# Optimization experiments

Hardware: AMD Instinct MI355X
Metric: run time of the kernel (lower is better)

Reference implementation:

```python
import jax, jax.numpy as jnp
import numpy as np

N_NODES = 100000
N_EDGES = 1600000
IN_DIM, HIDDEN_DIM, OUT_DIM = 64, 128, 40


def setup_inputs() -> dict:
    key = jax.random.key(0)
    k1, k2, k3, k4 = jax.random.split(key, 4)
    x = jax.random.normal(k1, (N_NODES, IN_DIM), dtype=jnp.float32)
    edge_index = jax.random.randint(k2, (2, N_EDGES), 0, N_NODES, dtype=jnp.int64)
    W1 = jax.random.normal(k3, (IN_DIM, HIDDEN_DIM), dtype=jnp.float32) * 0.05
    b1 = jnp.zeros((HIDDEN_DIM,), dtype=jnp.float32)
    W2 = jax.random.normal(k4, (HIDDEN_DIM, OUT_DIM), dtype=jnp.float32) * 0.05
    b2 = jnp.zeros((OUT_DIM,), dtype=jnp.float32)
    return {"x": x, "edge_index": edge_index, "W1": W1, "b1": b1, "W2": W2, "b2": b2}


def reference(x, edge_index, W1, b1, W2, b2):
    # PyG GINConv with default eps=0: out = nn(x_i + sum_{j in N(i)} x_j)
    src = edge_index[0]
    dst = edge_index[1]
    n = x.shape[0]

    def gin_layer(h, W, b):
        aggr = jax.ops.segment_sum(h[src], dst, num_segments=n)  # scatter-add of neighbor feats
        return (h + aggr) @ W + b

    h = jax.nn.relu(gin_layer(x, W1, b1))
    # dropout is identity in eval mode (training=False)
    h = gin_layer(h, W2, b2)
    return jax.nn.log_softmax(h, axis=1)
```

## Files before the change

### kernel.cpp

```cpp
#include <hip/hip_runtime.h>
#include <math.h>


#define IN_DIM 64
#define HID_DIM 128
#define OUT_DIM 40

#define BSH 8
#define MAXNB 512
#define EPB 4096
#define CAP 5120
#define H1S 136
#define EPT 16
#define CPT 20

typedef unsigned short ushort;
typedef unsigned char uchar;
typedef unsigned int uint;
typedef float floatx2 __attribute__((ext_vector_type(2)));
typedef short short8_t __attribute__((ext_vector_type(8)));
typedef float float4_t __attribute__((ext_vector_type(4)));

__device__ __forceinline__ ushort f2bf(float f) {
  unsigned u = __float_as_uint(f);
  u += 0x7fffu + ((u >> 16) & 1u);
  return (ushort)(u >> 16);
}


__global__ __launch_bounds__(256) void prep(
    const float4* __restrict__ x4, uint2* __restrict__ x8, int n8,
    const float* __restrict__ W1, const float* __restrict__ W2,
    ushort* __restrict__ W1T, ushort* __restrict__ W2T, int* __restrict__ gcur) {
  int id = blockIdx.x * 256 + threadIdx.x;
  if (id < n8) {
    float4 a = x4[2 * id], b = x4[2 * id + 1];
    int p0 = __builtin_amdgcn_cvt_pk_fp8_f32(a.x, a.y, 0, false);
    p0 = __builtin_amdgcn_cvt_pk_fp8_f32(a.z, a.w, p0, true);
    int p1 = __builtin_amdgcn_cvt_pk_fp8_f32(b.x, b.y, 0, false);
    p1 = __builtin_amdgcn_cvt_pk_fp8_f32(b.z, b.w, p1, true);
    x8[id] = (uint2){(uint)p0, (uint)p1};
  }
  if (id < HID_DIM * IN_DIM) {
    int c = id / IN_DIM, k = id - c * IN_DIM;
    W1T[id] = f2bf(W1[k * HID_DIM + c]);
  }
  if (id < 48 * HID_DIM) {
    int c = id / HID_DIM, k = id - c * HID_DIM;
    W2T[id] = (c < OUT_DIM) ? f2bf(W2[k * OUT_DIM + c]) : 0;
  }
  if (id < MAXNB) gcur[id] = 0;
}


__global__ __launch_bounds__(256) void bucket_scatter(
    const int* __restrict__ src, const int* __restrict__ dst,
    int* __restrict__ gcur, int* __restrict__ epk_s, int n_edges, int nb) {
  __shared__ int hist[MAXNB];
  __shared__ int lexcl[MAXNB];
  __shared__ int lofs[MAXNB];
  __shared__ int gbase[MAXNB];
  __shared__ int spk[EPB];
  __shared__ ushort sbid[EPB];
  int tid = threadIdx.x;
  for (int i = tid; i < nb; i += 256) { hist[i] = 0; lofs[i] = 0; }
  __syncthreads();
  int e0 = blockIdx.x * EPB;
  int cnt = min(EPB, n_edges - e0);
  int dr[EPT], sr[EPT];
#pragma unroll
  for (int r = 0; r < EPT; ++r) {
    int i = r * 256 + tid;
    if (i < cnt) {
      dr[r] = dst[e0 + i];
      sr[r] = src[e0 + i];
      atomicAdd(&hist[dr[r] >> BSH], 1);
    } else { dr[r] = -1; sr[r] = 0; }
  }
  __syncthreads();
  if (tid < 64) {
    int carry = 0;
    for (int c = 0; c < nb; c += 64) {
      int v = (c + tid < nb) ? hist[c + tid] : 0;
      int incl = v;
#pragma unroll
      for (int d = 1; d < 64; d <<= 1) {
        int t = __shfl_up(incl, d, 64);
        if (tid >= d) incl += t;
      }
      if (c + tid < nb) lexcl[c + tid] = carry + incl - v;
      carry += __shfl(incl, 63, 64);
    }
  }
  __syncthreads();
  for (int i = tid; i < nb; i += 256)
    if (hist[i]) gbase[i] = atomicAdd(&gcur[i], hist[i]);
  __syncthreads();
#pragma unroll
  for (int r = 0; r < EPT; ++r) {
    if (dr[r] >= 0) {
      int b = dr[r] >> BSH;
      int p = lexcl[b] + atomicAdd(&lofs[b], 1);
      spk[p] = ((dr[r] & 255) << 17) | sr[r];
      sbid[p] = (ushort)b;
    }
  }
  __syncthreads();
  for (int i = tid; i < cnt; i += 256) {
    int b = sbid[i];
    epk_s[b * CAP + gbase[b] + (i - lexcl[b])] = spk[i];
  }
}


__global__ __launch_bounds__(256) void bucket_csr(
    const int* __restrict__ epk_s, const int* __restrict__ gcnt,
    int2* __restrict__ off2, int* __restrict__ esrc_s, int n_nodes) {
  __shared__ int hist[256];
  __shared__ int cur[256];
  int b = blockIdx.x;
  int base = b * CAP;
  int cnt = gcnt[b];
  int nb0 = b << BSH;
  int nn = min(256, n_nodes - nb0);
  int tid = threadIdx.x;
  hist[tid] = 0;
  __syncthreads();
  int pv[CPT];
#pragma unroll
  for (int r = 0; r < CPT; ++r) {
    int i = r * 256 + tid;
    if (i < cnt) {
      pv[r] = epk_s[base + i];
      atomicAdd(&hist[pv[r] >> 17], 1);
    } else pv[r] = -1;
  }
  __syncthreads();
  if (tid < 64) {
    int carry = 0;
#pragma unroll
    for (int c = 0; c < 256; c += 64) {
      int v = hist[c + tid];
      int incl = v;
#pragma unroll
      for (int d = 1; d < 64; d <<= 1) {
        int t = __shfl_up(incl, d, 64);
        if (tid >= d) incl += t;
      }
      cur[c + tid] = carry + incl - v;
      carry += __shfl(incl, 63, 64);
    }
  }
  __syncthreads();
  if (tid < nn) {
    int st = cur[tid];
    off2[nb0 + tid] = make_int2(base + st, base + st + hist[tid]);
  }
  __syncthreads();
#pragma unroll
  for (int r = 0; r < CPT; ++r) {
    if (pv[r] >= 0) {
      int pos = atomicAdd(&cur[pv[r] >> 17], 1);
      esrc_s[base + pos] = pv[r] & 0x1FFFF;
    }
  }
}


__global__ __launch_bounds__(256) void agg1(
    const float4* __restrict__ x4, const uint2* __restrict__ x8,
    const int2* __restrict__ off2, const int* __restrict__ esrc,
    ushort* __restrict__ aggrh, int n_nodes) {
  int tid = threadIdx.x;
  int lane = tid & 63;
  int nsel = (lane >> 5) & 1, es = (lane >> 3) & 3, q = lane & 7;
  int node = blockIdx.x * 8 + (tid >> 6) * 2 + nsel;
  bool nok = node < n_nodes;
  int2 oe = nok ? off2[node] : make_int2(0, 0);
  floatx2 A0 = {0.f, 0.f}, A1 = {0.f, 0.f}, A2 = {0.f, 0.f}, A3 = {0.f, 0.f};
  floatx2 C0 = {0.f, 0.f}, C1 = {0.f, 0.f}, C2 = {0.f, 0.f}, C3 = {0.f, 0.f};
  int e = oe.x, end = oe.y;
  for (; e + 8 <= end; e += 8) {
    uint2 u0 = x8[(uint)(esrc[e + es] * 8 + q)];
    uint2 u1 = x8[(uint)(esrc[e + 4 + es] * 8 + q)];
    A0 += __builtin_amdgcn_cvt_pk_f32_fp8((int)u0.x, false);
    A1 += __builtin_amdgcn_cvt_pk_f32_fp8((int)u0.x, true);
    A2 += __builtin_amdgcn_cvt_pk_f32_fp8((int)u0.y, false);
    A3 += __builtin_amdgcn_cvt_pk_f32_fp8((int)u0.y, true);
    C0 += __builtin_amdgcn_cvt_pk_f32_fp8((int)u1.x, false);
    C1 += __builtin_amdgcn_cvt_pk_f32_fp8((int)u1.x, true);
    C2 += __builtin_amdgcn_cvt_pk_f32_fp8((int)u1.y, false);
    C3 += __builtin_amdgcn_cvt_pk_f32_fp8((int)u1.y, true);
  }
  for (; e < end; e += 4) {
    int idx = e + es;
    if (idx < end) {
      uint2 u = x8[(uint)(esrc[idx] * 8 + q)];
      A0 += __builtin_amdgcn_cvt_pk_f32_fp8((int)u.x, false);
      A1 += __builtin_amdgcn_cvt_pk_f32_fp8((int)u.x, true);
      A2 += __builtin_amdgcn_cvt_pk_f32_fp8((int)u.y, false);
      A3 += __builtin_amdgcn_cvt_pk_f32_fp8((int)u.y, true);
    }
  }
  A0 += C0; A1 += C1; A2 += C2; A3 += C3;
#pragma unroll
  for (int d = 8; d <= 16; d <<= 1) {
    floatx2 t0, t1, t2, t3;
    t0[0] = __shfl_xor(A0[0], d, 64); t0[1] = __shfl_xor(A0[1], d, 64);
    t1[0] = __shfl_xor(A1[0], d, 64); t1[1] = __shfl_xor(A1[1], d, 64);
    t2[0] = __shfl_xor(A2[0], d, 64); t2[1] = __shfl_xor(A2[1], d, 64);
    t3[0] = __shfl_xor(A3[0], d, 64); t3[1] = __shfl_xor(A3[1], d, 64);
    A0 += t0; A1 += t1; A2 += t2; A3 += t3;
  }
  if (nok) {
    float4 xa = x4[(uint)(node * 16 + q * 2)];
    float4 xb = x4[(uint)(node * 16 + q * 2 + 1)];
    A0 += (floatx2){xa.x, xa.y};
    A1 += (floatx2){xa.z, xa.w};
    A2 += (floatx2){xb.x, xb.y};
    A3 += (floatx2){xb.z, xb.w};
  }
  if (nok && es == 0) {
    uint4 o;
    o.x = (uint)f2bf(A0[0]) | ((uint)f2bf(A0[1]) << 16);
    o.y = (uint)f2bf(A1[0]) | ((uint)f2bf(A1[1]) << 16);
    o.z = (uint)f2bf(A2[0]) | ((uint)f2bf(A2[1]) << 16);
    o.w = (uint)f2bf(A3[0]) | ((uint)f2bf(A3[1]) << 16);
    ((uint4*)aggrh)[(uint)(node * 8 + q)] = o;
  }
}


__global__ __launch_bounds__(256) void gemm12_mfma(
    const ushort* __restrict__ aggrh, const ushort* __restrict__ W1T,
    const float* __restrict__ b1, const ushort* __restrict__ W2T,
    uchar* __restrict__ th8, int n_nodes) {
  __shared__ ushort h1s[64 * H1S];
  int w = threadIdx.x >> 6, lane = threadIdx.x & 63;
  int n0 = blockIdx.x * 64 + w * 16;
  int row = lane & 15, kg = lane >> 4;
  int n = n0 + row;
  {
    short8_t a0 = {}, a1 = {};
    if (n < n_nodes) {
      a0 = *(const short8_t*)&aggrh[(size_t)n * IN_DIM + kg * 8];
      a1 = *(const short8_t*)&aggrh[(size_t)n * IN_DIM + 32 + kg * 8];
    }
    float4_t acc[8];
#pragma unroll
    for (int ct = 0; ct < 8; ++ct) acc[ct] = (float4_t){0.f, 0.f, 0.f, 0.f};
#pragma unroll
    for (int ct = 0; ct < 8; ++ct) {
      int c = ct * 16 + row;
      short8_t b0 = *(const short8_t*)&W1T[(size_t)c * IN_DIM + kg * 8];
      short8_t b1f = *(const short8_t*)&W1T[(size_t)c * IN_DIM + 32 + kg * 8];
      acc[ct] = __builtin_amdgcn_mfma_f32_16x16x32_bf16(a0, b0, acc[ct], 0, 0, 0);
      acc[ct] = __builtin_amdgcn_mfma_f32_16x16x32_bf16(a1, b1f, acc[ct], 0, 0, 0);
    }
#pragma unroll
    for (int ct = 0; ct < 8; ++ct) {
      int j = ct * 16 + row;
      float bias = b1[j];
#pragma unroll
      for (int i = 0; i < 4; ++i) {
        int nl = w * 16 + kg * 4 + i;
        h1s[nl * H1S + j] = f2bf(fmaxf(acc[ct][i] + bias, 0.f));
      }
    }
  }
  __syncthreads();
  {
    short8_t a[4];
#pragma unroll
    for (int ks = 0; ks < 4; ++ks)
      a[ks] = *(const short8_t*)&h1s[(w * 16 + row) * H1S + ks * 32 + kg * 8];
    float4_t acc[3];
#pragma unroll
    for (int ct = 0; ct < 3; ++ct) acc[ct] = (float4_t){0.f, 0.f, 0.f, 0.f};
#pragma unroll
    for (int ct = 0; ct < 3; ++ct) {
      int c = ct * 16 + row;
#pragma unroll
      for (int ks = 0; ks < 4; ++ks) {
        short8_t b = *(const short8_t*)&W2T[(size_t)c * HID_DIM + ks * 32 + kg * 8];
        acc[ct] = __builtin_amdgcn_mfma_f32_16x16x32_bf16(a[ks], b, acc[ct], 0, 0, 0);
      }
    }
#pragma unroll
    for (int ct = 0; ct < 3; ++ct) {
      int j = ct * 16 + row;
      if (j < OUT_DIM) {
#pragma unroll
        for (int i = 0; i < 4; ++i) {
          int nn = n0 + kg * 4 + i;
          if (nn < n_nodes) {
            int pk = __builtin_amdgcn_cvt_pk_fp8_f32(acc[ct][i], acc[ct][i], 0, false);
            th8[(size_t)nn * 40 + j] = (uchar)(pk & 0xff);
          }
        }
      }
    }
  }
}


__global__ __launch_bounds__(256) void final_fused(
    const uchar* __restrict__ th8, const int2* __restrict__ off2,
    const int* __restrict__ esrc, const float* __restrict__ b2,
    float* __restrict__ out, int n_nodes) {
  int tid = threadIdx.x;
  int lane = tid & 63;
  int nsel = (lane >> 5) & 1, es = (lane >> 4) & 1, q = lane & 15;
  int node = blockIdx.x * 8 + (tid >> 6) * 2 + nsel;
  bool nok = node < n_nodes;
  bool valid = nok && (q < 10);
  const uint* tr = (const uint*)th8;
  int2 oe = nok ? off2[node] : make_int2(0, 0);
  uint uown = 0;
  float4 bb = {0.f, 0.f, 0.f, 0.f};
  if (valid) {
    uown = tr[(uint)(node * 10 + q)];
    bb = ((const float4*)b2)[q];
  }
  floatx2 A01 = {0.f, 0.f}, A23 = {0.f, 0.f};
  floatx2 C01 = {0.f, 0.f}, C23 = {0.f, 0.f};
  int e = oe.x, end = oe.y;
  for (; e + 8 <= end; e += 8) {
    uint u0 = 0, u1 = 0, u2 = 0, u3 = 0;
    if (valid) {
      u0 = tr[(uint)(esrc[e + es] * 10 + q)];
      u1 = tr[(uint)(esrc[e + es + 2] * 10 + q)];
      u2 = tr[(uint)(esrc[e + es + 4] * 10 + q)];
      u3 = tr[(uint)(esrc[e + es + 6] * 10 + q)];
    }
    A01 += __builtin_amdgcn_cvt_pk_f32_fp8((int)u0, false);
    A23 += __builtin_amdgcn_cvt_pk_f32_fp8((int)u0, true);
    C01 += __builtin_amdgcn_cvt_pk_f32_fp8((int)u1, false);
    C23 += __builtin_amdgcn_cvt_pk_f32_fp8((int)u1, true);
    A01 += __builtin_amdgcn_cvt_pk_f32_fp8((int)u2, false);
    A23 += __builtin_amdgcn_cvt_pk_f32_fp8((int)u2, true);
    C01 += __builtin_amdgcn_cvt_pk_f32_fp8((int)u3, false);
    C23 += __builtin_amdgcn_cvt_pk_f32_fp8((int)u3, true);
  }
  for (; e < end; e += 2) {
    int idx = e + es;
    if (idx < end && valid) {
      uint u = tr[(uint)(esrc[idx] * 10 + q)];
      A01 += __builtin_amdgcn_cvt_pk_f32_fp8((int)u, false);
      A23 += __builtin_amdgcn_cvt_pk_f32_fp8((int)u, true);
    }
  }
  A01 += C01; A23 += C23;
  {
    floatx2 t0, t1;
    t0[0] = __shfl_xor(A01[0], 16, 64); t0[1] = __shfl_xor(A01[1], 16, 64);
    t1[0] = __shfl_xor(A23[0], 16, 64); t1[1] = __shfl_xor(A23[1], 16, 64);
    A01 += t0; A23 += t1;
  }
  A01 += __builtin_amdgcn_cvt_pk_f32_fp8((int)uown, false);
  A23 += __builtin_amdgcn_cvt_pk_f32_fp8((int)uown, true);
  A01 += (floatx2){bb.x, bb.y};
  A23 += (floatx2){bb.z, bb.w};
  float m = valid ? fmaxf(fmaxf(A01[0], A01[1]), fmaxf(A23[0], A23[1])) : -INFINITY;
#pragma unroll
  for (int d = 1; d <= 8; d <<= 1) m = fmaxf(m, __shfl_xor(m, d, 64));
  float ssum = 0.f;
  if (valid)
    ssum = (__expf(A01[0] - m) + __expf(A01[1] - m)) +
           (__expf(A23[0] - m) + __expf(A23[1] - m));
#pragma unroll
  for (int d = 1; d <= 8; d <<= 1) ssum += __shfl_xor(ssum, d, 64);
  if (valid && es == 0) {
    float ls = m + __logf(ssum);
    float4 o = {A01[0] - ls, A01[1] - ls, A23[0] - ls, A23[1] - ls};
    ((float4*)out)[(uint)(node * 10 + q)] = o;
  }
}


static inline char* align256(char* p) {
  return (char*)(((uintptr_t)p + 255) & ~(uintptr_t)255);
}

extern "C" void kernel_launch(void* const* d_in, const int* in_sizes, int n_in,
                              void* d_out, int out_size, void* d_ws, size_t ws_size,
                              hipStream_t stream) {
  const float* x  = (const float*)d_in[0];
  const int*   ei = (const int*)d_in[1];
  const float* W1 = (const float*)d_in[2];
  const float* b1 = (const float*)d_in[3];
  const float* W2 = (const float*)d_in[4];
  const float* b2 = (const float*)d_in[5];
  float* out = (float*)d_out;

  int n_nodes = in_sizes[0] / IN_DIM;
  int n_edges = in_sizes[1] / 2;
  const int* src = ei;
  const int* dst = ei + n_edges;
  int nb = (n_nodes + 255) >> BSH;

  char* p = (char*)d_ws;
  int* gcur   = (int*)p;            p += MAXNB * 4;
  int2* off2  = (int2*)p;           p += (size_t)n_nodes * 8;
  p = align256(p);
  int* epk_s  = (int*)p;            p += (size_t)nb * CAP * 4;
  int* esrc_s = (int*)p;            p += (size_t)nb * CAP * 4;
  p = align256(p);
  uchar* x8    = (uchar*)p;         p += (size_t)n_nodes * IN_DIM;
  p = align256(p);
  ushort* aggrh = (ushort*)p;       p += (size_t)n_nodes * IN_DIM * 2;
  p = align256(p);
  uchar* th8    = (uchar*)p;        p += (size_t)n_nodes * 40 + 256;
  p = align256(p);
  ushort* W1T   = (ushort*)p;       p += HID_DIM * IN_DIM * 2;
  ushort* W2T   = (ushort*)p;       p += 48 * HID_DIM * 2;

  int n8 = n_nodes * IN_DIM / 8;
  prep<<<(n8 + 255) / 256, 256, 0, stream>>>(
      (const float4*)x, (uint2*)x8, n8, W1, W2, W1T, W2T, gcur);

  int egrid = (n_edges + EPB - 1) / EPB;
  bucket_scatter<<<egrid, 256, 0, stream>>>(src, dst, gcur, epk_s, n_edges, nb);
  bucket_csr<<<nb, 256, 0, stream>>>(epk_s, gcur, off2, esrc_s, n_nodes);

  agg1<<<(n_nodes + 7) / 8, 256, 0, stream>>>(
      (const float4*)x, (const uint2*)x8, off2, esrc_s, aggrh, n_nodes);
  int ggrid = (n_nodes + 63) / 64;
  gemm12_mfma<<<ggrid, 256, 0, stream>>>(aggrh, W1T, b1, W2T, th8, n_nodes);
  final_fused<<<(n_nodes + 7) / 8, 256, 0, stream>>>(th8, off2, esrc_s, b2, out, n_nodes);
}
```

Before: 138.1 us.

## Scatter bucketed edges directly to global and widen fp8 gathers in final layer

The bucket scatter kernel no longer stages edges in shared memory with a local prefix scan. It writes each packed edge straight to its global bucket slot using a per-block global base plus a shared atomic offset, which removes a scan, two barriers and the LDS staging at the cost of less coalesced global writes. The final aggregation kernel now has each lane load 8 fp8 bytes (uint2) instead of 4 and processes 4 edges in parallel per node instead of 2, so fewer lanes sit idle (5 of 8 valid instead of 10 of 16). This adds an extra shuffle reduction stage.

Measured after the change: 139.1 us. No clear change (+0.7%).

```diff
diff --git a/kernel.cpp b/kernel.cpp
--- a/kernel.cpp
+++ b/kernel.cpp
@@ -57,11 +57,8 @@
     const int* __restrict__ src, const int* __restrict__ dst,
     int* __restrict__ gcur, int* __restrict__ epk_s, int n_edges, int nb) {
   __shared__ int hist[MAXNB];
-  __shared__ int lexcl[MAXNB];
   __shared__ int lofs[MAXNB];
   __shared__ int gbase[MAXNB];
-  __shared__ int spk[EPB];
-  __shared__ ushort sbid[EPB];
   int tid = threadIdx.x;
   for (int i = tid; i < nb; i += 256) { hist[i] = 0; lofs[i] = 0; }
   __syncthreads();
@@ -78,21 +75,6 @@
     } else { dr[r] = -1; sr[r] = 0; }
   }
   __syncthreads();
-  if (tid < 64) {
-    int carry = 0;
-    for (int c = 0; c < nb; c += 64) {
-      int v = (c + tid < nb) ? hist[c + tid] : 0;
-      int incl = v;
-#pragma unroll
-      for (int d = 1; d < 64; d <<= 1) {
-        int t = __shfl_up(incl, d, 64);
-        if (tid >= d) incl += t;
-      }
-      if (c + tid < nb) lexcl[c + tid] = carry + incl - v;
-      carry += __shfl(incl, 63, 64);
-    }
-  }
-  __syncthreads();
   for (int i = tid; i < nb; i += 256)
     if (hist[i]) gbase[i] = atomicAdd(&gcur[i], hist[i]);
   __syncthreads();
@@ -100,15 +82,9 @@
   for (int r = 0; r < EPT; ++r) {
     if (dr[r] >= 0) {
       int b = dr[r] >> BSH;
-      int p = lexcl[b] + atomicAdd(&lofs[b], 1);
-      spk[p] = ((dr[r] & 255) << 17) | sr[r];
-      sbid[p] = (ushort)b;
-    }
-  }
-  __syncthreads();
-  for (int i = tid; i < cnt; i += 256) {
-    int b = sbid[i];
-    epk_s[b * CAP + gbase[b] + (i - lexcl[b])] = spk[i];
+      int p = gbase[b] + atomicAdd(&lofs[b], 1);
+      epk_s[b * CAP + p] = ((dr[r] & 255) << 17) | sr[r];
+    }
   }
 }
 
@@ -310,70 +286,84 @@
     float* __restrict__ out, int n_nodes) {
   int tid = threadIdx.x;
   int lane = tid & 63;
-  int nsel = (lane >> 5) & 1, es = (lane >> 4) & 1, q = lane & 15;
+  int nsel = (lane >> 5) & 1, es = (lane >> 3) & 3, q = lane & 7;
   int node = blockIdx.x * 8 + (tid >> 6) * 2 + nsel;
   bool nok = node < n_nodes;
-  bool valid = nok && (q < 10);
-  const uint* tr = (const uint*)th8;
+  bool valid = nok && (q < 5);
+  const uint2* tr2 = (const uint2*)th8;
   int2 oe = nok ? off2[node] : make_int2(0, 0);
-  uint uown = 0;
-  float4 bb = {0.f, 0.f, 0.f, 0.f};
+  uint2 uown = {0, 0};
+  float4 bb0 = {0.f, 0.f, 0.f, 0.f}, bb1 = {0.f, 0.f, 0.f, 0.f};
   if (valid) {
-    uown = tr[(uint)(node * 10 + q)];
-    bb = ((const float4*)b2)[q];
-  }
-  floatx2 A01 = {0.f, 0.f}, A23 = {0.f, 0.f};
-  floatx2 C01 = {0.f, 0.f}, C23 = {0.f, 0.f};
+    uown = tr2[(uint)(node * 5 + q)];
+    bb0 = ((const float4*)b2)[2 * q];
+    bb1 = ((const float4*)b2)[2 * q + 1];
+  }
+  floatx2 A0 = {0.f, 0.f}, A1 = {0.f, 0.f}, A2 = {0.f, 0.f}, A3 = {0.f, 0.f};
+  floatx2 C0 = {0.f, 0.f}, C1 = {0.f, 0.f}, C2 = {0.f, 0.f}, C3 = {0.f, 0.f};
   int e = oe.x, end = oe.y;
   for (; e + 8 <= end; e += 8) {
-    uint u0 = 0, u1 = 0, u2 = 0, u3 = 0;
+    uint2 u0 = {0, 0}, u1 = {0, 0};
     if (valid) {
-      u0 = tr[(uint)(esrc[e + es] * 10 + q)];
-      u1 = tr[(uint)(esrc[e + es + 2] * 10 + q)];
-      u2 = tr[(uint)(esrc[e + es + 4] * 10 + q)];
-      u3 = tr[(uint)(esrc[e + es + 6] * 10 + q)];
-    }
-    A01 += __builtin_amdgcn_cvt_pk_f32_fp8((int)u0, false);
-    A23 += __builtin_amdgcn_cvt_pk_f32_fp8((int)u0, true);
-    C01 += __builtin_amdgcn_cvt_pk_f32_fp8((int)u1, false);
-    C23 += __builtin_amdgcn_cvt_pk_f32_fp8((int)u1, true);
-    A01 += __builtin_amdgcn_cvt_pk_f32_fp8((int)u2, false);
-    A23 += __builtin_amdgcn_cvt_pk_f32_fp8((int)u2, true);
-    C01 += __builtin_amdgcn_cvt_pk_f32_fp8((int)u3, false);
-    C23 += __builtin_amdgcn_cvt_pk_f32_fp8((int)u3, true);
-  }
-  for (; e < end; e += 2) {
+      u0 = tr2[(uint)(esrc[e + es] * 5 + q)];
+      u1 = tr2[(uint)(esrc[e + 4 + es] * 5 + q)];
+    }
+    A0 += __builtin_amdgcn_cvt_pk_f32_fp8((int)u0.x, false);
+    A1 += __builtin_amdgcn_cvt_pk_f32_fp8((int)u0.x, true);
+    A2 += __builtin_amdgcn_cvt_pk_f32_fp8((int)u0.y, false);
+    A3 += __builtin_amdgcn_cvt_pk_f32_fp8((int)u0.y, true);
+    C0 += __builtin_amdgcn_cvt_pk_f32_fp8((int)u1.x, false);
+    C1 += __builtin_amdgcn_cvt_pk_f32_fp8((int)u1.x, true);
+    C2 += __builtin_amdgcn_cvt_pk_f32_fp8((int)u1.y, false);
+    C3 += __builtin_amdgcn_cvt_pk_f32_fp8((int)u1.y, true);
+  }
+  for (; e < end; e += 4) {
     int idx = e + es;
     if (idx < end && valid) {
-      uint u = tr[(uint)(esrc[idx] * 10 + q)];
-      A01 += __builtin_amdgcn_cvt_pk_f32_fp8((int)u, false);
-      A23 += __builtin_amdgcn_cvt_pk_f32_fp8((int)u, true);
-    }
-  }
-  A01 += C01; A23 += C23;
-  {
-    floatx2 t0, t1;
-    t0[0] = __shfl_xor(A01[0], 16, 64); t0[1] = __shfl_xor(A01[1], 16, 64);
-    t1[0] = __shfl_xor(A23[0], 16, 64); t1[1] = __shfl_xor(A23[1], 16, 64);
-    A01 += t0; A23 += t1;
-  }
-  A01 += __builtin_amdgcn_cvt_pk_f32_fp8((int)uown, false);
-  A23 += __builtin_amdgcn_cvt_pk_f32_fp8((int)uown, true);
-  A01 += (floatx2){bb.x, bb.y};
-  A23 += (floatx2){bb.z, bb.w};
-  float m = valid ? fmaxf(fmaxf(A01[0], A01[1]), fmaxf(A23[0], A23[1])) : -INFINITY;
-#pragma unroll
-  for (int d = 1; d <= 8; d <<= 1) m = fmaxf(m, __shfl_xor(m, d, 64));
+      uint2 u = tr2[(uint)(esrc[idx] * 5 + q)];
+      A0 += __builtin_amdgcn_cvt_pk_f32_fp8((int)u.x, false);
+      A1 += __builtin_amdgcn_cvt_pk_f32_fp8((int)u.x, true);
+      A2 += __builtin_amdgcn_cvt_pk_f32_fp8((int)u.y, false);
+      A3 += __builtin_amdgcn_cvt_pk_f32_fp8((int)u.y, true);
+    }
+  }
+  A0 += C0; A1 += C1; A2 += C2; A3 += C3;
+#pragma unroll
+  for (int d = 8; d <= 16; d <<= 1) {
+    floatx2 t0, t1, t2, t3;
+    t0[0] = __shfl_xor(A0[0], d, 64); t0[1] = __shfl_xor(A0[1], d, 64);
+    t1[0] = __shfl_xor(A1[0], d, 64); t1[1] = __shfl_xor(A1[1], d, 64);
+    t2[0] = __shfl_xor(A2[0], d, 64); t2[1] = __shfl_xor(A2[1], d, 64);
+    t3[0] = __shfl_xor(A3[0], d, 64); t3[1] = __shfl_xor(A3[1], d, 64);
+    A0 += t0; A1 += t1; A2 += t2; A3 += t3;
+  }
+  A0 += __builtin_amdgcn_cvt_pk_f32_fp8((int)uown.x, false);
+  A1 += __builtin_amdgcn_cvt_pk_f32_fp8((int)uown.x, true);
+  A2 += __builtin_amdgcn_cvt_pk_f32_fp8((int)uown.y, false);
+  A3 += __builtin_amdgcn_cvt_pk_f32_fp8((int)uown.y, true);
+  A0 += (floatx2){bb0.x, bb0.y};
+  A1 += (floatx2){bb0.z, bb0.w};
+  A2 += (floatx2){bb1.x, bb1.y};
+  A3 += (floatx2){bb1.z, bb1.w};
+  float m = valid ? fmaxf(fmaxf(fmaxf(A0[0], A0[1]), fmaxf(A1[0], A1[1])),
+                          fmaxf(fmaxf(A2[0], A2[1]), fmaxf(A3[0], A3[1])))
+                  : -INFINITY;
+#pragma unroll
+  for (int d = 1; d <= 4; d <<= 1) m = fmaxf(m, __shfl_xor(m, d, 64));
   float ssum = 0.f;
   if (valid)
-    ssum = (__expf(A01[0] - m) + __expf(A01[1] - m)) +
-           (__expf(A23[0] - m) + __expf(A23[1] - m));
-#pragma unroll
-  for (int d = 1; d <= 8; d <<= 1) ssum += __shfl_xor(ssum, d, 64);
+    ssum = ((__expf(A0[0] - m) + __expf(A0[1] - m)) +
+            (__expf(A1[0] - m) + __expf(A1[1] - m))) +
+           ((__expf(A2[0] - m) + __expf(A2[1] - m)) +
+            (__expf(A3[0] - m) + __expf(A3[1] - m)));
+#pragma unroll
+  for (int d = 1; d <= 4; d <<= 1) ssum += __shfl_xor(ssum, d, 64);
   if (valid && es == 0) {
     float ls = m + __logf(ssum);
-    float4 o = {A01[0] - ls, A01[1] - ls, A23[0] - ls, A23[1] - ls};
-    ((float4*)out)[(uint)(node * 10 + q)] = o;
+    float4 o0 = {A0[0] - ls, A0[1] - ls, A1[0] - ls, A1[1] - ls};
+    float4 o1 = {A2[0] - ls, A2[1] - ls, A3[0] - ls, A3[1] - ls};
+    ((float4*)out)[(uint)(node * 10 + 2 * q)] = o0;
+    ((float4*)out)[(uint)(node * 10 + 2 * q + 1)] = o1;
   }
 }
 
```
